# Kernel tuning notes

Measured on AMD Instinct MI355X. Metric: run time of the kernel, lower is better.

Reference implementation:

```python
import jax, jax.numpy as jnp
import numpy as np

B, S, D_TEXT, MAXF = 2, 1024, 384, 5
D_MODEL, N_HEADS, D_FF, L = 768, 12, 3072, 4
HEAD_DIM = D_MODEL // N_HEADS
EPS = 1e-6
NEG = -1e9


def _rms(x, g):
    return x * jax.lax.rsqrt(jnp.mean(x * x, axis=-1, keepdims=True) + EPS) * g


def _attn(x, w, mask):
    # w: [4, d, d] = (wq, wk, wv, wo); mask: [b, s, s] bool (True = attend)
    b, s, d = x.shape

    def proj(W):
        return jnp.einsum('bsd,de->bse', x, W).reshape(b, s, N_HEADS, HEAD_DIM).transpose(0, 2, 1, 3)

    q, k, v = proj(w[0]), proj(w[1]), proj(w[2])
    scale = jnp.asarray(1.0 / np.sqrt(HEAD_DIM), x.dtype)
    scores = jnp.einsum('bhqe,bhke->bhqk', q, k) * scale
    scores = jnp.where(mask[:, None], scores, NEG)
    p = jax.nn.softmax(scores, axis=-1)
    o = jnp.einsum('bhqk,bhke->bhqe', p, v).transpose(0, 2, 1, 3).reshape(b, s, d)
    return jnp.einsum('bsd,de->bse', o, w[3])


def _forward(number_values, datetime_values, boolean_values, text_values, column_name_values,
             W_cn, b_cn, W_num, b_num, W_text, b_text, W_dt, b_dt, W_bool, b_bool,
             g_cn, g_num, g_text, g_dt, g_bool, mask_emb,
             blk_norms, blk_attn, blk_up, blk_gate, blk_down,
             g_out, Wd_num, bd_num, Wd_dt, bd_dt, Wd_bool, bd_bool, Wd_text, bd_text,
             node_indices, table_name_indices, column_name_indices,
             f2p_neighbor_indices, semantic_types, masks, is_padding):
    valid = ~is_padding
    pv = valid[:, :, None] & valid[:, None, :]  # [b,s,s]
    eye = jnp.eye(S, dtype=bool)[None]
    same_node = node_indices[:, :, None] == node_indices[:, None, :]
    col_mask = ((column_name_indices[:, :, None] == column_name_indices[:, None, :])
                & (table_name_indices[:, :, None] == table_name_indices[:, None, :]) & pv) | eye
    feat_mask = (same_node & pv) | eye
    # kv node is one of q's f2p neighbors
    nei = (f2p_neighbor_indices[:, :, :, None] == node_indices[:, None, None, :]).any(axis=2)
    nei_mask = ((nei | same_node) & pv) | eye
    full_mask = pv | eye

    # per-semantic-type value encoders (Linear + RMSNorm)
    cn = _rms(column_name_values @ W_cn + b_cn, g_cn)
    num_e = _rms(number_values @ W_num + b_num, g_num)
    text_e = _rms(text_values @ W_text + b_text, g_text)
    dt_e = _rms(datetime_values @ W_dt + b_dt, g_dt)
    bool_e = _rms(boolean_values @ W_bool + b_bool, g_bool)
    st = semantic_types[..., None]
    val = jnp.where(st == 0, num_e, jnp.where(st == 1, text_e, jnp.where(st == 2, dt_e, bool_e)))
    # masked cells get the learned mask embedding for their semantic type
    val = jnp.where(masks[..., None], mask_emb[semantic_types], val)
    x = val + cn

    for i in range(L):
        nw, aw = blk_norms[i], blk_attn[i]
        x = x + _attn(_rms(x, nw[0]), aw[0], col_mask)
        x = x + _attn(_rms(x, nw[1]), aw[1], feat_mask)
        x = x + _attn(_rms(x, nw[2]), aw[2], nei_mask)
        x = x + _attn(_rms(x, nw[3]), aw[3], full_mask)
        h = _rms(x, nw[4])
        x = x + (jax.nn.silu(h @ blk_gate[i]) * (h @ blk_up[i])) @ blk_down[i]

    h = _rms(x, g_out)
    return (h @ Wd_num + bd_num, h @ Wd_dt + bd_dt, h @ Wd_bool + bd_bool, h @ Wd_text + bd_text)


def setup_inputs() -> dict:
    key = jax.random.key(0)
    ks = iter(jax.random.split(key, 64))

    def nrm(shape, scale=0.02):
        return jax.random.normal(next(ks), shape, jnp.float32) * scale

    inp = {}
    inp['number_values'] = jax.random.normal(next(ks), (B, S, 1), jnp.float32)
    inp['datetime_values'] = jax.random.normal(next(ks), (B, S, 1), jnp.float32)
    inp['boolean_values'] = jax.random.normal(next(ks), (B, S, 1), jnp.float32)
    inp['text_values'] = jax.random.normal(next(ks), (B, S, D_TEXT), jnp.float32)
    inp['column_name_values'] = jax.random.normal(next(ks), (B, S, D_TEXT), jnp.float32)
    inp['W_cn'] = nrm((D_TEXT, D_MODEL)); inp['b_cn'] = jnp.zeros((D_MODEL,), jnp.float32)
    inp['W_num'] = nrm((1, D_MODEL)); inp['b_num'] = jnp.zeros((D_MODEL,), jnp.float32)
    inp['W_text'] = nrm((D_TEXT, D_MODEL)); inp['b_text'] = jnp.zeros((D_MODEL,), jnp.float32)
    inp['W_dt'] = nrm((1, D_MODEL)); inp['b_dt'] = jnp.zeros((D_MODEL,), jnp.float32)
    inp['W_bool'] = nrm((1, D_MODEL)); inp['b_bool'] = jnp.zeros((D_MODEL,), jnp.float32)
    for n in ('g_cn', 'g_num', 'g_text', 'g_dt', 'g_bool'):
        inp[n] = jnp.ones((D_MODEL,), jnp.float32)
    inp['mask_emb'] = jax.random.normal(next(ks), (4, D_MODEL), jnp.float32)
    inp['blk_norms'] = jnp.ones((L, 5, D_MODEL), jnp.float32)
    inp['blk_attn'] = nrm((L, 4, 4, D_MODEL, D_MODEL))
    inp['blk_up'] = nrm((L, D_MODEL, D_FF))
    inp['blk_gate'] = nrm((L, D_MODEL, D_FF))
    inp['blk_down'] = nrm((L, D_FF, D_MODEL))
    inp['g_out'] = jnp.ones((D_MODEL,), jnp.float32)
    inp['Wd_num'] = nrm((D_MODEL, 1)); inp['bd_num'] = jnp.zeros((1,), jnp.float32)
    inp['Wd_dt'] = nrm((D_MODEL, 1)); inp['bd_dt'] = jnp.zeros((1,), jnp.float32)
    inp['Wd_bool'] = nrm((D_MODEL, 1)); inp['bd_bool'] = jnp.zeros((1,), jnp.float32)
    inp['Wd_text'] = nrm((D_MODEL, D_TEXT)); inp['bd_text'] = jnp.zeros((D_TEXT,), jnp.float32)
    inp['node_indices'] = jax.random.randint(next(ks), (B, S), 0, 128)
    inp['table_name_indices'] = jax.random.randint(next(ks), (B, S), 0, 8)
    inp['column_name_indices'] = jax.random.randint(next(ks), (B, S), 0, 32)
    inp['f2p_neighbor_indices'] = jax.random.randint(next(ks), (B, S, MAXF), 0, 128)
    inp['semantic_types'] = jax.random.randint(next(ks), (B, S), 0, 4)
    inp['masks'] = jax.random.bernoulli(next(ks), 0.15, (B, S))
    inp['is_padding'] = jnp.zeros((B, S), bool)
    return inp


def reference(number_values, datetime_values, boolean_values, text_values, column_name_values,
              W_cn, b_cn, W_num, b_num, W_text, b_text, W_dt, b_dt, W_bool, b_bool,
              g_cn, g_num, g_text, g_dt, g_bool, mask_emb,
              blk_norms, blk_attn, blk_up, blk_gate, blk_down,
              g_out, Wd_num, bd_num, Wd_dt, bd_dt, Wd_bool, bd_bool, Wd_text, bd_text,
              node_indices, table_name_indices, column_name_indices,
              f2p_neighbor_indices, semantic_types, masks, is_padding):
    return _forward(number_values, datetime_values, boolean_values, text_values, column_name_values,
                    W_cn, b_cn, W_num, b_num, W_text, b_text, W_dt, b_dt, W_bool, b_bool,
                    g_cn, g_num, g_text, g_dt, g_bool, mask_emb,
                    blk_norms, blk_attn, blk_up, blk_gate, blk_down,
                    g_out, Wd_num, bd_num, Wd_dt, bd_dt, Wd_bool, bd_bool, Wd_text, bd_text,
                    node_indices, table_name_indices, column_name_indices,
                    f2p_neighbor_indices, semantic_types, masks, is_padding)
```

## Files before the change

kernel.cpp:

```cpp
#include <hip/hip_runtime.h>
#include <hip/hip_bf16.h>
#include <cmath>
#include <stdint.h>


#define BB 2
#define SS 1024
#define DT 384
#define DM 768
#define NH 12
#define DH 64
#define DFF 3072
#define NL 4
#define NROW (BB*SS)
#define EPSF 1e-6f
#define QSC 0.1803368801111244f

typedef unsigned short u16;
typedef unsigned char u8;
typedef unsigned int u32;
typedef __attribute__((ext_vector_type(8))) short s16x8;
typedef __attribute__((ext_vector_type(4))) float f32x4;

__device__ __forceinline__ u16 f2bu(float f){
    u32 x = __float_as_uint(f);
    u32 r = (x + 0x7fffu + ((x>>16)&1u)) >> 16;
    return (u16)r;
}
__device__ __forceinline__ u32 pk2(float lo, float hi){
    return (u32)f2bu(lo) | ((u32)f2bu(hi)<<16);
}
__device__ __forceinline__ int swz(int row, int c){
    return (row<<6) + (((((c>>3) ^ row) & 7))<<3) + (c&7);
}
__device__ __forceinline__ float rsum16(float v){
    v += __shfl_xor(v,1); v += __shfl_xor(v,2);
    v += __shfl_xor(v,4); v += __shfl_xor(v,8);
    return v;
}
#define SBAR() __builtin_amdgcn_sched_barrier(0)
#define GLDS(src,dst) __builtin_amdgcn_global_load_lds((const __attribute__((address_space(1))) u32*)(src), (__attribute__((address_space(3))) u32*)(dst), 16, 0, 0)
#define GLDS4(src,dst) __builtin_amdgcn_global_load_lds((const __attribute__((address_space(1))) u32*)(src), (__attribute__((address_space(3))) u32*)(dst), 4, 0, 0)

__device__ void norm_bool_body(const void* __restrict__ src, u8* __restrict__ dst, int n)
{
    __shared__ int fl[4];
    if (threadIdx.x<4) fl[threadIdx.x]=0;
    __syncthreads();
    const u32* wsrc = (const u32*)src;
    const int nw = n/4;
    int any=0, nb=0, hi=0, lo=0;
    for (int i=threadIdx.x;i<nw;i+=blockDim.x){
        u32 v=wsrc[i];
        if (!v) continue;
        any=1;
        #pragma unroll
        for (int b=0;b<4;b++){
            u32 by=(v>>(8*b))&0xffu;
            if (by>1u) nb=1;
            if (by==1u && b!=0) hi=1;
        }
        if ((v&0xffffu)==0x3f80u) lo=1;
    }
    if (any) atomicOr(&fl[0],1);
    if (nb)  atomicOr(&fl[1],1);
    if (hi)  atomicOr(&fl[2],1);
    if (lo)  atomicOr(&fl[3],1);
    __syncthreads();
    int c;
    if (!fl[0]) c=0;
    else if (!fl[1]) c = fl[2] ? 2 : 1;
    else if (fl[3]) c = 3;
    else c = 1;
    for (int i=threadIdx.x;i<n;i+=blockDim.x){
        u8 v;
        if (c==0)      v=0;
        else if (c==1) v = (((const u32*)src)[i]!=0u);
        else if (c==2) v = (((const u8*)src)[i]!=0u);
        else           v = (((const u16*)src)[i]!=0u);
        dst[i]=v;
    }
}
__global__ void norm_bool2(const void* s0, u8* d0, const void* s1, u8* d1, int n)
{
    if (blockIdx.x==0) norm_bool_body(s0,d0,n);
    else               norm_bool_body(s1,d1,n);
}

__global__ void pack_meta(const int* __restrict__ node, const int* __restrict__ colx,
                          const int* __restrict__ tbl, const u8* __restrict__ pad,
                          u32* __restrict__ pm, int n, float* __restrict__ rsz, int nz)
{
    int i = blockIdx.x*256 + threadIdx.x;
    if (i<n)
        pm[i] = (u32)(node[i]&0xff) | ((u32)(colx[i]&0xff)<<8) | ((u32)(tbl[i]&0xff)<<16) | ((u32)(pad[i]&1)<<24);
    for (int z=i; z<nz; z+=gridDim.x*256) rsz[z]=0.f;
}

__global__ __launch_bounds__(256) void mask4_kernel(const u32* __restrict__ pm, const int* __restrict__ f2p,
                                                    u8* __restrict__ m4)
{
    const int b = blockIdx.y, kg = blockIdx.x;
    const int t = threadIdx.x;
    __shared__ u32 qm[1024];
    __shared__ int qf[1024*5];
    for (int i=t;i<1024;i+=256) qm[i] = pm[b*SS+i];
    for (int i=t;i<5*1024;i+=256) qf[i] = f2p[b*SS*5 + i];
    __syncthreads();
    const int q0 = t*4;
    u32 qmv[4]; int qn[4]; int qfv[4][5];
    #pragma unroll
    for (int j=0;j<4;j++){
        qmv[j]=qm[q0+j]; qn[j]=(int)(qmv[j]&0xffu);
        #pragma unroll
        for (int f=0;f<5;f++) qfv[j][f]=qf[(q0+j)*5+f];
    }
    for (int kk=0;kk<16;kk++){
        const int k = kg*16+kk;
        const u32 km = qm[k];
        const int kn = (int)(km&0xffu);
        u32 outw=0;
        #pragma unroll
        for (int j=0;j<4;j++){
            const u32 qmw = qmv[j];
            const bool pv = (((qmw|km)>>24)&1u)==0u;
            u32 by=0;
            if ((((qmw^km)&0x00ffff00u)==0u) && pv) by|=1;
            if ((((qmw^km)&0xffu)==0u) && pv) by|=2;
            bool nei = (qfv[j][0]==kn)||(qfv[j][1]==kn)||(qfv[j][2]==kn)||(qfv[j][3]==kn)||(qfv[j][4]==kn)
                       ||(qn[j]==kn);
            if (nei && pv) by|=4;
            if (pv) by|=8;
            if ((q0+j)==k) by=15;
            outw |= by<<(8*j);
        }
        ((u32*)(m4 + ((size_t)b<<20) + ((size_t)k<<10)))[t] = outw;
    }
}

__global__ void repack_mask(const u8* __restrict__ m4, u8* __restrict__ mbp)
{
    const int gid = blockIdx.x*256 + threadIdx.x;
    const int qb = gid & 127;
    const int bk = gid >> 7;
    const u8* src = m4 + ((size_t)bk<<10) + qb*8;
    u32 lo = *(const u32*)src, hi = *(const u32*)(src+4);
    u32 out[4] = {0,0,0,0};
    #pragma unroll
    for (int j=0;j<4;j++){
        u32 b0 = (lo>>(8*j)) & 0xffu;
        u32 b1 = (hi>>(8*j)) & 0xffu;
        #pragma unroll
        for (int tt=0;tt<4;tt++){
            out[tt] |= ((b0>>tt)&1u) << j;
            out[tt] |= ((b1>>tt)&1u) << (j+4);
        }
    }
    u8* dst = mbp + (size_t)bk*512 + qb;
    #pragma unroll
    for (int tt=0;tt<4;tt++) dst[tt*128] = (u8)out[tt];
}

__global__ __launch_bounds__(256) void transpose_cvt2(const float* __restrict__ src, u16* __restrict__ dst,
                                                      int K, int N, size_t dz,
                                                      const float* __restrict__ gbase, int gmode)
{
    const int z = blockIdx.z;
    src += (size_t)z*K*N;
    dst += (size_t)z*dz;
    const float* g = nullptr;
    if (gmode==1){ int m = z&3; if (m<3) g = gbase + (size_t)((z>>4)*5 + ((z>>2)&3))*768; }
    else if (gmode==2){ g = gbase + (size_t)z*5*768; }
    const int n0 = blockIdx.x*32, k0 = blockIdx.y*64;
    __shared__ float t[64][33];
    const int tid = threadIdx.x;
    const int kr = tid>>3, n4 = (tid&7)*4;
    #pragma unroll
    for (int p=0;p<2;p++){
        const int k = p*32 + kr;
        float gk = g ? g[k0+k] : 1.f;
        float4 v = *(const float4*)(src + (size_t)(k0+k)*N + n0 + n4);
        t[k][n4]=v.x*gk; t[k][n4+1]=v.y*gk; t[k][n4+2]=v.z*gk; t[k][n4+3]=v.w*gk;
    }
    __syncthreads();
    const int n = tid>>3, ks = (tid&7)*8;
    const int ng = n0 + n;
    uint4 o;
    u32* op = (u32*)&o;
    #pragma unroll
    for (int i=0;i<4;i++)
        op[i] = pk2(t[ks+2*i][n], t[ks+2*i+1][n]);
    *(uint4*)&dst[(((size_t)(ng>>7)*(K>>6) + (k0>>6))<<13) + ((ng&127)<<6) + ks] = o;
}

__global__ __launch_bounds__(256) void cvt_tiled2(const float* __restrict__ s0, u16* __restrict__ d0,
                                                  const float* __restrict__ s1, u16* __restrict__ d1, int K)
{
    const float* src = blockIdx.y ? s1 : s0;
    u16* dst = blockIdx.y ? d1 : d0;
    const int gid = blockIdx.x*256 + threadIdx.x;
    const int base = gid*8;
    const int row = base / K, col = base - row*K;
    float4 a = *(const float4*)(src + base);
    float4 b = *(const float4*)(src + base + 4);
    uint4 o;
    o.x = pk2(a.x,a.y); o.y = pk2(a.z,a.w);
    o.z = pk2(b.x,b.y); o.w = pk2(b.z,b.w);
    *(uint4*)&dst[(((size_t)(row>>7)*(K>>6) + (col>>6))<<13) + ((row&127)<<6) + (col&63)] = o;
}

__device__ __forceinline__ void stage3(const u16* aT, const u16* bT, int cb, int brow,
                                       u16* la, u16* lb, int w, int l)
{
    #pragma unroll
    for (int p=0;p<2;p++){
        const int q = p*256 + w*64 + l;
        const int row = q>>2, u = q&3;
        const int so = row*64 + cb + (((u ^ ((row>>1)&3))&3)<<3);
        GLDS(aT+so, la + p*2048 + w*512);
    }
    {
        const int q = w*64 + l;
        const int row = q>>2, u = q&3;
        const int so = (brow+row)*64 + cb + (((u ^ ((row>>1)&3))&3)<<3);
        GLDS(bT+so, lb + w*512);
    }
}

__global__ __launch_bounds__(256,3) void gemm_t(
    const u16* __restrict__ At, const u16* __restrict__ Bt,
    int K, int AMS, u16* __restrict__ qk16, u16* __restrict__ vt16,
    const float* __restrict__ rs_in)
{
    __shared__ u16 lds[4][6144];
    const int tid = threadIdx.x;
    const int lane = tid & 63, w = tid >> 6;
    const int cg = lane >> 4, cl = lane & 15;
    const int NT = K >> 5;
    const int n0 = blockIdx.x*64;
    const int brow = n0 & 64;
    const size_t bNb = (size_t)(n0>>7)*(K>>6);

    const u16* aB = At + ((size_t)blockIdx.y * AMS << 13);
    const u16* bB = Bt + (bNb << 13);

    f32x4 acc[2][4];
    #pragma unroll
    for (int i=0;i<2;i++)
        #pragma unroll
        for (int j=0;j<4;j++) acc[i][j] = (f32x4){0.f,0.f,0.f,0.f};

    stage3(aB, bB, 0,  brow, &lds[0][0], &lds[0][4096], w, lane);
    stage3(aB, bB, 32, brow, &lds[1][0], &lds[1][4096], w, lane);

    for (int kt=0; kt<NT; kt++){
        const int buf = kt & 3;
        if (kt+2 < NT){
            const int k2 = kt+2;
            stage3(aB + ((size_t)(k2>>1)<<13), bB + ((size_t)(k2>>1)<<13),
                   (k2&1)<<5, brow, &lds[k2&3][0], &lds[k2&3][4096], w, lane);
            asm volatile("s_waitcnt vmcnt(6)" ::: "memory");
        } else if (kt+1 < NT){
            asm volatile("s_waitcnt vmcnt(3)" ::: "memory");
        } else {
            asm volatile("s_waitcnt vmcnt(0)" ::: "memory");
        }
        SBAR(); __builtin_amdgcn_s_barrier(); SBAR();
        s16x8 af[2], bf[4];
        #pragma unroll
        for (int mt=0;mt<2;mt++){
            const int ra = w*32 + mt*16 + cl;
            af[mt] = *(const s16x8*)&lds[buf][ra*32 + (((cg ^ ((ra>>1)&3))&3)<<3)];
        }
        #pragma unroll
        for (int nt=0;nt<4;nt++){
            const int rb = nt*16 + cl;
            bf[nt] = *(const s16x8*)&lds[buf][4096 + rb*32 + (((cg ^ ((rb>>1)&3))&3)<<3)];
        }
        #pragma unroll
        for (int mt=0;mt<2;mt++)
            #pragma unroll
            for (int nt=0;nt<4;nt++)
                acc[mt][nt] = __builtin_amdgcn_mfma_f32_16x16x32_bf16(af[mt], bf[nt], acc[mt][nt], 0,0,0);
    }

    const int m0 = blockIdx.y*128;
    #pragma unroll
    for (int mt=0;mt<2;mt++){
        const int grow0 = m0 + w*32 + mt*16 + cg*4;
        float rr[4];
        #pragma unroll
        for (int j=0;j<4;j++) rr[j] = rsqrtf(rs_in[grow0+j]*(1.f/768.f) + EPSF);
        #pragma unroll
        for (int nt=0;nt<4;nt++){
            const int col = n0 + nt*16 + cl;
            if (col < 768){
                #pragma unroll
                for (int j=0;j<4;j++)
                    qk16[(size_t)(grow0+j)*1536 + col] = f2bu(acc[mt][nt][j]*rr[j]*QSC);
            } else if (col < 1536){
                #pragma unroll
                for (int j=0;j<4;j++)
                    qk16[(size_t)(grow0+j)*1536 + col] = f2bu(acc[mt][nt][j]*rr[j]);
            } else {
                const int b = grow0>>10, s0 = grow0&1023;
                const int dhg = col - 1536;
                uint2 o;
                o.x = pk2(acc[mt][nt][0]*rr[0], acc[mt][nt][1]*rr[1]);
                o.y = pk2(acc[mt][nt][2]*rr[2], acc[mt][nt][3]*rr[3]);
                *(uint2*)(vt16 + ((size_t)(b*768 + dhg)<<10) + s0) = o;
            }
        }
    }
}

__global__ __launch_bounds__(256,3) void gemm_gu(
    const u16* __restrict__ At, const u16* __restrict__ Bg, const u16* __restrict__ Bu,
    const float* __restrict__ rs_in, u16* __restrict__ o16)
{
    __shared__ u16 lds[3][8192];
    const int tid = threadIdx.x;
    const int lane = tid & 63, w = tid >> 6;
    const int cg = lane >> 4, cl = lane & 15;
    const int NT = 24;
    const int n0 = blockIdx.x*64;
    const int brow = n0 & 64;
    const size_t bNb = (size_t)(n0>>7)*12;

    const u16* aB = At + ((size_t)blockIdx.y * 12 << 13);
    const u16* gB = Bg + (bNb << 13);
    const u16* uB = Bu + (bNb << 13);

    f32x4 accg[2][4], accu[2][4];
    #pragma unroll
    for (int i=0;i<2;i++)
        #pragma unroll
        for (int j=0;j<4;j++){ accg[i][j] = (f32x4){0.f,0.f,0.f,0.f}; accu[i][j] = (f32x4){0.f,0.f,0.f,0.f}; }

    #define STAGE_GU(kt2, cb, buf) { \
        const u16* a_ = aB + ((size_t)(kt2)<<13); \
        const u16* g_ = gB + ((size_t)(kt2)<<13); \
        const u16* u_ = uB + ((size_t)(kt2)<<13); \
        _Pragma("unroll") \
        for (int p=0;p<2;p++){ \
            const int q = p*256 + w*64 + lane; \
            const int row = q>>2, uu = q&3; \
            const int so = row*64 + (cb) + (((uu ^ ((row>>1)&3))&3)<<3); \
            GLDS(a_+so, &lds[buf][0] + p*2048 + w*512); \
        } \
        { \
            const int q = w*64 + lane; \
            const int row = q>>2, uu = q&3; \
            const int so = (brow+row)*64 + (cb) + (((uu ^ ((row>>1)&3))&3)<<3); \
            GLDS(g_+so, &lds[buf][4096] + w*512); \
            GLDS(u_+so, &lds[buf][6144] + w*512); \
        } }

    STAGE_GU(0, 0, 0);

    for (int kt=0; kt<NT; kt++){
        const int buf = kt % 3;
        if (kt+1 < NT){
            const int k1 = kt+1;
            STAGE_GU(k1>>1, (k1&1)<<5, k1%3);
            asm volatile("s_waitcnt vmcnt(4)" ::: "memory");
        } else {
            asm volatile("s_waitcnt vmcnt(0)" ::: "memory");
        }
        SBAR(); __builtin_amdgcn_s_barrier(); SBAR();
        s16x8 af[2], bg[4], bu[4];
        #pragma unroll
        for (int mt=0;mt<2;mt++){
            const int ra = w*32 + mt*16 + cl;
            af[mt] = *(const s16x8*)&lds[buf][ra*32 + (((cg ^ ((ra>>1)&3))&3)<<3)];
        }
        #pragma unroll
        for (int nt=0;nt<4;nt++){
            const int rb = nt*16 + cl;
            const int sw = (((cg ^ ((rb>>1)&3))&3)<<3);
            bg[nt] = *(const s16x8*)&lds[buf][4096 + rb*32 + sw];
            bu[nt] = *(const s16x8*)&lds[buf][6144 + rb*32 + sw];
        }
        #pragma unroll
        for (int mt=0;mt<2;mt++)
            #pragma unroll
            for (int nt=0;nt<4;nt++){
                accg[mt][nt] = __builtin_amdgcn_mfma_f32_16x16x32_bf16(af[mt], bg[nt], accg[mt][nt], 0,0,0);
                accu[mt][nt] = __builtin_amdgcn_mfma_f32_16x16x32_bf16(af[mt], bu[nt], accu[mt][nt], 0,0,0);
            }
    }

    const int m0 = blockIdx.y*128;
    #pragma unroll
    for (int mt=0;mt<2;mt++){
        const int grow0 = m0 + w*32 + mt*16 + cg*4;
        float rr[4];
        #pragma unroll
        for (int j=0;j<4;j++) rr[j] = rsqrtf(rs_in[grow0+j]*(1.f/768.f) + EPSF);
        #pragma unroll
        for (int nt=0;nt<4;nt++){
            const int col = n0 + nt*16 + cl;
            const size_t tb = (((size_t)(grow0>>7)*48 + (col>>6))<<13) + (col&63);
            #pragma unroll
            for (int j=0;j<4;j++){
                float g = accg[mt][nt][j]*rr[j];
                float u = accu[mt][nt][j]*rr[j];
                float s = g/(1.f+__expf(-g))*u;
                o16[tb + (((grow0+j)&127)<<6)] = f2bu(s);
            }
        }
    }
}

__device__ __forceinline__ void stage64(const u16* aT, int arow, const u16* bT, int brow, int cb,
                                        u16* la, u16* lb, int w, int l)
{
    const int q = w*64 + l;
    const int row = q>>2, u = q&3;
    const int sw = (((u ^ ((row>>1)&3))&3)<<3);
    GLDS(aT + (arow+row)*64 + cb + sw, la + w*512);
    GLDS(bT + (brow+row)*64 + cb + sw, lb + w*512);
}

__global__ __launch_bounds__(256,4) void gemm_t64(
    const u16* __restrict__ At, const u16* __restrict__ Bt, float* __restrict__ C,
    int N, int K, int AMS, int flags, const float* __restrict__ bias,
    u16* __restrict__ o16, float* __restrict__ rs_out)
{
    __shared__ u16 lds[4][4096];
    const int tid = threadIdx.x;
    const int lane = tid & 63, w = tid >> 6;
    const int cg = lane >> 4, cl = lane & 15;
    const int NT = K >> 5;
    const int n0 = blockIdx.x*64;
    const int m0 = blockIdx.y*64;
    const int brow = n0 & 64, arow = m0 & 64;

    const u16* aB = At + ((size_t)(m0>>7) * AMS << 13);
    const u16* bB = Bt + ((size_t)(n0>>7) * (K>>6) << 13);

    f32x4 acc[4];
    #pragma unroll
    for (int j=0;j<4;j++) acc[j] = (f32x4){0.f,0.f,0.f,0.f};

    stage64(aB, arow, bB, brow, 0,  &lds[0][0], &lds[0][2048], w, lane);
    stage64(aB, arow, bB, brow, 32, &lds[1][0], &lds[1][2048], w, lane);

    for (int kt=0; kt<NT; kt++){
        const int buf = kt & 3;
        if (kt+2 < NT){
            const int k2 = kt+2;
            stage64(aB + ((size_t)(k2>>1)<<13), arow, bB + ((size_t)(k2>>1)<<13), brow,
                    (k2&1)<<5, &lds[k2&3][0], &lds[k2&3][2048], w, lane);
            asm volatile("s_waitcnt vmcnt(4)" ::: "memory");
        } else if (kt+1 < NT){
            asm volatile("s_waitcnt vmcnt(2)" ::: "memory");
        } else {
            asm volatile("s_waitcnt vmcnt(0)" ::: "memory");
        }
        SBAR(); __builtin_amdgcn_s_barrier(); SBAR();
        const int ra = w*16 + cl;
        s16x8 af = *(const s16x8*)&lds[buf][ra*32 + (((cg ^ ((ra>>1)&3))&3)<<3)];
        s16x8 bf[4];
        #pragma unroll
        for (int nt=0;nt<4;nt++){
            const int rb = nt*16 + cl;
            bf[nt] = *(const s16x8*)&lds[buf][2048 + rb*32 + (((cg ^ ((rb>>1)&3))&3)<<3)];
        }
        #pragma unroll
        for (int nt=0;nt<4;nt++)
            acc[nt] = __builtin_amdgcn_mfma_f32_16x16x32_bf16(af, bf[nt], acc[nt], 0,0,0);
    }

    const int grow0 = m0 + w*16 + cg*4;
    const bool do_acc = (flags&1), do_bias = (flags&2);
    float tmp[4][4];
    #pragma unroll
    for (int nt=0;nt<4;nt++){
        const int col = n0 + nt*16 + cl;
        float bv = do_bias ? bias[col] : 0.f;
        #pragma unroll
        for (int j=0;j<4;j++){
            float v = acc[nt][j] + bv;
            float* cp = C + (size_t)(grow0+j)*N + col;
            if (do_acc) v += *cp;
            *cp = v;
            tmp[nt][j] = v;
        }
    }
    if (o16){
        #pragma unroll
        for (int nt=0;nt<4;nt++){
            const int col = n0 + nt*16 + cl;
            const size_t tb = (((size_t)(grow0>>7)*12 + (col>>6))<<13) + (col&63);
            #pragma unroll
            for (int j=0;j<4;j++)
                o16[tb + (((grow0+j)&127)<<6)] = f2bu(tmp[nt][j]);
        }
    }
    if (rs_out){
        #pragma unroll
        for (int j=0;j<4;j++){
            float s = tmp[0][j]*tmp[0][j] + tmp[1][j]*tmp[1][j]
                    + tmp[2][j]*tmp[2][j] + tmp[3][j]*tmp[3][j];
            s = rsum16(s);
            if (cl==0) atomicAdd(rs_out + grow0 + j, s);
        }
    }
}

__global__ __launch_bounds__(256,2) void attn_mfma5(
    const u16* __restrict__ qk16, const u16* __restrict__ vt16,
    const u8* __restrict__ mbp, int mt,
    u16* __restrict__ ob16)
{
    const int bh = blockIdx.y;
    const int b = bh / NH, h = bh % NH;
    const int q0 = blockIdx.x * 64;
    const int tid = threadIdx.x;
    const int w = tid>>6, lane = tid&63, cg = lane>>4, cl = lane&15;
    const int srow = lane>>3;
    const int sseg = (lane&7) ^ srow;

    __shared__ u16 Ks[3][4096], Vt[3][4096], Ps[4096];
    __shared__ u8 Ms[3][512];

    s16x8 qa0, qa1;
    {
        const u16* qrow = qk16 + (size_t)(b*SS+q0 + w*16 + cl)*1536 + h*64;
        qa0 = *(const s16x8*)(qrow + cg*8);
        qa1 = *(const s16x8*)(qrow + 32 + cg*8);
        asm volatile("" :: "v"(*(const f32x4*)&qa0), "v"(*(const f32x4*)&qa1));
    }

    const u16* kbase = qk16 + (size_t)(b*SS)*1536 + 768 + h*64;
    const u16* vbase = vt16 + ((size_t)(b*768 + h*64)<<10);
    const u8* mrow0 = mbp + ((size_t)(b<<10))*512 + mt*128 + (q0>>3);

    #pragma unroll
    for (int p=0;p<2;p++){
        const int row = p*32 + w*8 + srow;
        GLDS(kbase + (size_t)row*1536 + sseg*8, Ks[0] + p*2048 + w*512);
        GLDS(vbase + ((size_t)row<<10) + sseg*8, Vt[0] + p*2048 + w*512);
    }
    if (lane < 32){
        const int krow = w*16 + (lane>>1);
        GLDS4(mrow0 + (size_t)krow*512 + (lane&1)*4, Ms[0] + w*128);
    }

    f32x4 o[4];
    #pragma unroll
    for (int nt=0;nt<4;nt++) o[nt] = (f32x4){0.f,0.f,0.f,0.f};
    float lsum[4] = {0.f,0.f,0.f,0.f};

    for (int kc=0;kc<16;kc++){
        const int buf = kc % 3;
        if (kc < 15){
            const int nb = (kc+1) % 3;
            const int kn0 = kc*64 + 64;
            #pragma unroll
            for (int p=0;p<2;p++){
                const int row = p*32 + w*8 + srow;
                GLDS(kbase + (size_t)(kn0+row)*1536 + sseg*8, Ks[nb] + p*2048 + w*512);
                GLDS(vbase + ((size_t)row<<10) + kn0 + sseg*8, Vt[nb] + p*2048 + w*512);
            }
            if (lane < 32){
                const int krow = kn0 + w*16 + (lane>>1);
                GLDS4(mrow0 + (size_t)krow*512 + (lane&1)*4, Ms[nb] + w*128);
            }
            asm volatile("s_waitcnt vmcnt(5)" ::: "memory");
        } else {
            asm volatile("s_waitcnt vmcnt(0)" ::: "memory");
        }
        SBAR(); __builtin_amdgcn_s_barrier(); SBAR();

        f32x4 sc[4];
        #pragma unroll
        for (int nt=0;nt<4;nt++) sc[nt] = (f32x4){0.f,0.f,0.f,0.f};
        __builtin_amdgcn_s_setprio(1);
        #pragma unroll
        for (int nt=0;nt<4;nt++){
            s16x8 kb0 = *(const s16x8*)&Ks[buf][swz(nt*16+cl, cg*8)];
            sc[nt] = __builtin_amdgcn_mfma_f32_16x16x32_bf16(qa0, kb0, sc[nt], 0,0,0);
        }
        #pragma unroll
        for (int nt=0;nt<4;nt++){
            s16x8 kb1 = *(const s16x8*)&Ks[buf][swz(nt*16+cl, 32+cg*8)];
            sc[nt] = __builtin_amdgcn_mfma_f32_16x16x32_bf16(qa1, kb1, sc[nt], 0,0,0);
        }
        __builtin_amdgcn_s_setprio(0);

        float pP[4][4];
        const int qb = 2*w + (cg>>1);
        const int bsh = (cg&1)*4;
        #pragma unroll
        for (int nt=0;nt<4;nt++){
            const u32 mrow = Ms[buf][(nt*16+cl)*8 + qb];
            #pragma unroll
            for (int j=0;j<4;j++){
                float pe = exp2f(fminf(sc[nt][j], 100.f));
                pe = ((mrow >> (bsh+j)) & 1u) ? pe : 0.f;
                pP[nt][j] = pe;
                lsum[j] += pe;
            }
        }

        #pragma unroll
        for (int nt=0;nt<4;nt++)
            #pragma unroll
            for (int j=0;j<4;j++)
                Ps[swz(w*16+cg*4+j, nt*16+cl)] = f2bu(pP[nt][j]);

        __builtin_amdgcn_s_setprio(1);
        #pragma unroll
        for (int ks=0;ks<2;ks++){
            s16x8 pa = *(const s16x8*)&Ps[swz(w*16+cl, ks*32+cg*8)];
            #pragma unroll
            for (int nt=0;nt<4;nt++){
                s16x8 vb = *(const s16x8*)&Vt[buf][swz(nt*16+cl, ks*32+cg*8)];
                o[nt] = __builtin_amdgcn_mfma_f32_16x16x32_bf16(pa, vb, o[nt], 0,0,0);
            }
        }
        __builtin_amdgcn_s_setprio(0);
    }

    #pragma unroll
    for (int j=0;j<4;j++){
        const float inv = 1.f/rsum16(lsum[j]);
        const int row = b*SS + q0 + w*16 + cg*4 + j;
        const size_t rb = ((size_t)(row>>7)*12 + h)*8192 + ((row&127)<<6);
        #pragma unroll
        for (int nt=0;nt<4;nt++)
            ob16[rb + nt*16 + cl] = f2bu(o[nt][j]*inv);
    }
}

__global__ __launch_bounds__(256) void fuse_encode(
    const float* __restrict__ cnbuf, const float* __restrict__ textbuf,
    const float* __restrict__ numv, const float* __restrict__ dtv, const float* __restrict__ boolv,
    const float* __restrict__ Wnum, const float* __restrict__ bnum,
    const float* __restrict__ Wdt, const float* __restrict__ bdt,
    const float* __restrict__ Wbool, const float* __restrict__ bbool,
    const float* __restrict__ gcn, const float* __restrict__ gnum, const float* __restrict__ gtext,
    const float* __restrict__ gdt, const float* __restrict__ gbool,
    const float* __restrict__ memb, const int* __restrict__ stypes, const u8* __restrict__ masks,
    float* __restrict__ x, u16* __restrict__ xt16, float* __restrict__ rs0)
{
    const int row = blockIdx.x;
    const int t = threadIdx.x;
    __shared__ float red[256];

    float cn3[3]; float ss=0.f;
    #pragma unroll
    for (int j=0;j<3;j++){
        cn3[j] = cnbuf[(size_t)row*DM + t + j*256];
        ss += cn3[j]*cn3[j];
    }
    red[t]=ss; __syncthreads();
    for (int s=128;s>0;s>>=1){ if(t<s) red[t]+=red[t+s]; __syncthreads(); }
    {
        float r = rsqrtf(red[0]/(float)DM + EPSF);
        #pragma unroll
        for (int j=0;j<3;j++) cn3[j] *= r*gcn[t+j*256];
    }
    __syncthreads();

    const int st = stypes[row];
    float val[3]; ss=0.f;
    if (st==1){
        #pragma unroll
        for (int j=0;j<3;j++){
            val[j] = textbuf[(size_t)row*DM + t + j*256];
            ss += val[j]*val[j];
        }
    } else {
        const float* Wp = (st==0)?Wnum:((st==2)?Wdt:Wbool);
        const float* bp = (st==0)?bnum:((st==2)?bdt:bbool);
        const float* vp = (st==0)?numv:((st==2)?dtv:boolv);
        float v = vp[row];
        #pragma unroll
        for (int j=0;j<3;j++){
            int e=t+j*256;
            val[j] = v*Wp[e] + bp[e];
            ss += val[j]*val[j];
        }
    }
    red[t]=ss; __syncthreads();
    for (int s=128;s>0;s>>=1){ if(t<s) red[t]+=red[t+s]; __syncthreads(); }
    const float* gp = (st==0)?gnum:((st==1)?gtext:((st==2)?gdt:gbool));
    float r2 = rsqrtf(red[0]/(float)DM + EPSF);
    bool mk = masks[row]!=0;
    float xv[3]; float sx=0.f;
    #pragma unroll
    for (int j=0;j<3;j++){
        int e=t+j*256;
        float vv = val[j]*r2*gp[e];
        if (mk) vv = memb[st*DM+e];
        xv[j] = vv + cn3[j];
        x[(size_t)row*DM+e] = xv[j];
        sx += xv[j]*xv[j];
    }
    __syncthreads();
    red[t]=sx; __syncthreads();
    for (int s=128;s>0;s>>=1){ if(t<s) red[t]+=red[t+s]; __syncthreads(); }
    if (t==0) rs0[row] = red[0];
    const size_t mb = (size_t)(row>>7)*12;
    const int rr = (row&127)<<6;
    #pragma unroll
    for (int j=0;j<3;j++){
        const int c = t + j*256;
        xt16[((mb + (c>>6))<<13) + rr + (c&63)] = f2bu(xv[j]);
    }
}

__global__ __launch_bounds__(256) void decode2(
    const float* __restrict__ x, const float* __restrict__ gout,
    const float* __restrict__ Wn, const float* __restrict__ bn,
    const float* __restrict__ Wd, const float* __restrict__ bd,
    const float* __restrict__ Wb, const float* __restrict__ bb,
    float* __restrict__ out, u16* __restrict__ h16)
{
    const int row = blockIdx.x;
    const int t = threadIdx.x;
    __shared__ float h[DM];
    __shared__ float red[256];
    const float* xr = x + (size_t)row*DM;
    float v0=xr[t], v1=xr[t+256], v2=xr[t+512];
    red[t]=v0*v0+v1*v1+v2*v2; __syncthreads();
    for (int s=128;s>0;s>>=1){ if(t<s) red[t]+=red[t+s]; __syncthreads(); }
    float r = rsqrtf(red[0]/(float)DM + EPSF);
    float h0 = v0*r*gout[t], h1 = v1*r*gout[t+256], h2 = v2*r*gout[t+512];
    h[t]=h0; h[t+256]=h1; h[t+512]=h2;
    const size_t mb = (size_t)(row>>7)*12;
    const int rr = (row&127)<<6;
    #pragma unroll
    for (int j=0;j<3;j++){
        const int c = t + j*256;
        const float v = (j==0?h0:(j==1?h1:h2));
        h16[((mb + (c>>6))<<13) + rr + (c&63)] = f2bu(v);
    }
    __syncthreads();

    float pn=0.f,pd=0.f,pb=0.f;
    for (int k=t;k<DM;k+=256){ float hv=h[k]; pn+=hv*Wn[k]; pd+=hv*Wd[k]; pb+=hv*Wb[k]; }
    red[t]=pn; __syncthreads();
    for (int s=128;s>0;s>>=1){ if(t<s) red[t]+=red[t+s]; __syncthreads(); }
    float tn=red[0]; __syncthreads();
    red[t]=pd; __syncthreads();
    for (int s=128;s>0;s>>=1){ if(t<s) red[t]+=red[t+s]; __syncthreads(); }
    float td=red[0]; __syncthreads();
    red[t]=pb; __syncthreads();
    for (int s=128;s>0;s>>=1){ if(t<s) red[t]+=red[t+s]; __syncthreads(); }
    float tb=red[0];
    if (t==0){
        out[row]          = tn + bn[0];
        out[NROW + row]   = td + bd[0];
        out[2*NROW + row] = tb + bb[0];
    }
}

extern "C" void kernel_launch(void* const* d_in, const int* in_sizes, int n_in,
                              void* d_out, int out_size, void* d_ws, size_t ws_size,
                              hipStream_t stream)
{
    const float* numv   = (const float*)d_in[0];
    const float* dtval  = (const float*)d_in[1];
    const float* boolv  = (const float*)d_in[2];
    const float* textv  = (const float*)d_in[3];
    const float* cnamev = (const float*)d_in[4];
    const float* Wcn=(const float*)d_in[5];  const float* bcn=(const float*)d_in[6];
    const float* Wnum=(const float*)d_in[7]; const float* bnum=(const float*)d_in[8];
    const float* Wtext=(const float*)d_in[9];const float* btext=(const float*)d_in[10];
    const float* Wdt=(const float*)d_in[11]; const float* bdt=(const float*)d_in[12];
    const float* Wbool=(const float*)d_in[13];const float* bbool=(const float*)d_in[14];
    const float* gcn=(const float*)d_in[15]; const float* gnum=(const float*)d_in[16];
    const float* gtext=(const float*)d_in[17];const float* gdt=(const float*)d_in[18];
    const float* gbool=(const float*)d_in[19];
    const float* memb=(const float*)d_in[20];
    const float* norms_all=(const float*)d_in[21];
    const float* attw_all=(const float*)d_in[22];
    const float* up_all=(const float*)d_in[23];
    const float* gate_all=(const float*)d_in[24];
    const float* down_all=(const float*)d_in[25];
    const float* gout=(const float*)d_in[26];
    const float* Wdn=(const float*)d_in[27]; const float* bdn=(const float*)d_in[28];
    const float* Wdd=(const float*)d_in[29]; const float* bdd=(const float*)d_in[30];
    const float* Wdb=(const float*)d_in[31]; const float* bdb=(const float*)d_in[32];
    const float* Wdtx=(const float*)d_in[33];const float* bdtx=(const float*)d_in[34];
    const int* node=(const int*)d_in[35];
    const int* tbl =(const int*)d_in[36];
    const int* colx=(const int*)d_in[37];
    const int* f2p =(const int*)d_in[38];
    const int* styp=(const int*)d_in[39];

    const size_t SA = (size_t)768*768;
    const size_t SG = (size_t)768*3072;
    const size_t SC = (size_t)384*768;
    const size_t NX = (size_t)NROW*DM;

    u8* base = (u8*)d_ws;
    float* x  = (float*)base;
    u16* xt16 = (u16*)(base + 6291456);
    u16* ob16 = (u16*)(base + 9437184);
    u16* qk16 = (u16*)(base + 12582912);
    u16* vt16 = (u16*)(base + 18874368);
    u16* gu16 = (u16*)(base + 22020096);
    u16* wA   = (u16*)(base + 47185920);
    u16* wGU  = wA + 64*SA;
    u16* wD   = wGU + 8*SG;
    u16* wCN  = wD + 4*SG;
    u16* wTX  = wCN + SC;
    u16* wDX  = wTX + SC;
    u8* nmask = (u8*)(wDX + SC);
    u8* npad  = nmask + NROW;
    u32* pmeta = (u32*)(npad + NROW + 64);
    float* rsbuf = (float*)(pmeta + NROW);
    u8* m4 = (u8*)(rsbuf + 21*2048);
    u8* mbp = m4 + ((size_t)2<<20);

    u16* cnT16   = qk16;
    u16* textT16 = vt16;
    float* cnbuf   = (float*)gu16;
    float* textbuf = cnbuf + NX;

    float* out = (float*)d_out;

    norm_bool2<<<2,256,0,stream>>>(d_in[40], nmask, d_in[41], npad, NROW);
    pack_meta<<<8,256,0,stream>>>(node, colx, tbl, npad, pmeta, NROW, rsbuf, 21*2048);
    mask4_kernel<<<dim3(64,2),256,0,stream>>>(pmeta, f2p, m4);
    repack_mask<<<1024,256,0,stream>>>(m4, mbp);

    transpose_cvt2<<<dim3(24,12,64),256,0,stream>>>(attw_all, wA, 768, 768, SA, norms_all, 1);
    transpose_cvt2<<<dim3(96,12,4),256,0,stream>>>(gate_all, wGU,      768, 3072, 2*SG, norms_all + 4*768, 2);
    transpose_cvt2<<<dim3(96,12,4),256,0,stream>>>(up_all,   wGU + SG, 768, 3072, 2*SG, norms_all + 4*768, 2);
    transpose_cvt2<<<dim3(24,48,4),256,0,stream>>>(down_all, wD, 3072, 768, SG, nullptr, 0);
    transpose_cvt2<<<dim3(24,6,1),256,0,stream>>>(Wcn,   wCN, 384, 768, 0, nullptr, 0);
    transpose_cvt2<<<dim3(24,6,1),256,0,stream>>>(Wtext, wTX, 384, 768, 0, nullptr, 0);
    transpose_cvt2<<<dim3(12,12,1),256,0,stream>>>(Wdtx, wDX, 768, 384, 0, nullptr, 0);

    cvt_tiled2<<<dim3(384,2),256,0,stream>>>(cnamev, cnT16, textv, textT16, 384);
    gemm_t64<<<dim3(12,32),256,0,stream>>>(cnT16,   wCN, cnbuf,   768, 384, 6, 2, bcn,   nullptr, nullptr);
    gemm_t64<<<dim3(12,32),256,0,stream>>>(textT16, wTX, textbuf, 768, 384, 6, 2, btext, nullptr, nullptr);
    fuse_encode<<<NROW,256,0,stream>>>(cnbuf, textbuf, numv, dtval, boolv,
        Wnum,bnum,Wdt,bdt,Wbool,bbool, gcn,gnum,gtext,gdt,gbool,
        memb, styp, nmask, x, xt16, rsbuf);

    const dim3 ga(SS/64, BB*NH);
    for (int l=0; l<NL; l++){
        for (int a=0; a<4; a++){
            const int slot = l*5 + a;
            const u16* wqkv = wA + (size_t)((l*4+a)*4)*SA;
            gemm_t<<<dim3(36,16),256,0,stream>>>(xt16, wqkv, 768, 12, qk16, vt16,
                rsbuf + (size_t)slot*2048);
            attn_mfma5<<<ga,256,0,stream>>>(qk16, vt16, mbp, a, ob16);
            gemm_t64<<<dim3(12,32),256,0,stream>>>(ob16, wqkv + 3*SA, x, 768, 768, 12, 1, nullptr,
                xt16, rsbuf + (size_t)(slot+1)*2048);
        }
        gemm_gu<<<dim3(48,16),256,0,stream>>>(xt16, wGU + (size_t)l*2*SG, wGU + (size_t)l*2*SG + SG,
            rsbuf + (size_t)(l*5+4)*2048, gu16);
        gemm_t64<<<dim3(12,32),256,0,stream>>>(gu16, wD + (size_t)l*SG, x, 768, 3072, 48, 1, nullptr,
            xt16, rsbuf + (size_t)((l+1)*5)*2048);
    }

    decode2<<<NROW,256,0,stream>>>(x, gout, Wdn,bdn, Wdd,bdd, Wdb,bdb, out, xt16);
    gemm_t64<<<dim3(6,32),256,0,stream>>>(xt16, wDX, out + 3*NROW, 384, 768, 12, 2, bdtx,
        nullptr, nullptr);
}
```

Measured before the change: 1.345 ms.

## Fuse mask bit-packing into mask kernel and deepen gate/up GEMM prefetch

The mask kernel now bit-packs its per-query mask bytes directly into the bit-plane layout, using a lane shuffle to merge neighbouring threads' words. This removes the separate repack kernel and the 2 MB intermediate mask buffer round-trip. Separately, the gate/up GEMM now prefetches two k-tiles ahead in its triple buffer instead of one, and adds a trailing barrier to protect buffer reuse. The deeper prefetch hides more load latency but costs an extra barrier on every iteration.

```diff
diff --git a/kernel.cpp b/kernel.cpp
--- a/kernel.cpp
+++ b/kernel.cpp
@@ -98,7 +98,7 @@
 }
 
 __global__ __launch_bounds__(256) void mask4_kernel(const u32* __restrict__ pm, const int* __restrict__ f2p,
-                                                    u8* __restrict__ m4)
+                                                    u8* __restrict__ mbp)
 {
     const int b = blockIdx.y, kg = blockIdx.x;
     const int t = threadIdx.x;
@@ -115,6 +115,8 @@
         #pragma unroll
         for (int f=0;f<5;f++) qfv[j][f]=qf[(q0+j)*5+f];
     }
+    const int qb = t>>1;
+    const bool hiHalf = (t&1);
     for (int kk=0;kk<16;kk++){
         const int k = kg*16+kk;
         const u32 km = qm[k];
@@ -134,31 +136,21 @@
             if ((q0+j)==k) by=15;
             outw |= by<<(8*j);
         }
-        ((u32*)(m4 + ((size_t)b<<20) + ((size_t)k<<10)))[t] = outw;
-    }
-}
-
-__global__ void repack_mask(const u8* __restrict__ m4, u8* __restrict__ mbp)
-{
-    const int gid = blockIdx.x*256 + threadIdx.x;
-    const int qb = gid & 127;
-    const int bk = gid >> 7;
-    const u8* src = m4 + ((size_t)bk<<10) + qb*8;
-    u32 lo = *(const u32*)src, hi = *(const u32*)(src+4);
-    u32 out[4] = {0,0,0,0};
-    #pragma unroll
-    for (int j=0;j<4;j++){
-        u32 b0 = (lo>>(8*j)) & 0xffu;
-        u32 b1 = (hi>>(8*j)) & 0xffu;
-        #pragma unroll
-        for (int tt=0;tt<4;tt++){
-            out[tt] |= ((b0>>tt)&1u) << j;
-            out[tt] |= ((b1>>tt)&1u) << (j+4);
-        }
-    }
-    u8* dst = mbp + (size_t)bk*512 + qb;
-    #pragma unroll
-    for (int tt=0;tt<4;tt++) dst[tt*128] = (u8)out[tt];
+        const u32 pw = __shfl_xor(outw, 1);
+        if (!hiHalf){
+            u8* dst = mbp + ((size_t)((b<<10)+k))*512 + qb;
+            #pragma unroll
+            for (int tt=0;tt<4;tt++){
+                u32 lo4=0, hi4=0;
+                #pragma unroll
+                for (int j=0;j<4;j++){
+                    lo4 |= ((outw>>(8*j+tt))&1u) << j;
+                    hi4 |= ((pw  >>(8*j+tt))&1u) << j;
+                }
+                dst[tt*128] = (u8)(lo4 | (hi4<<4));
+            }
+        }
+    }
 }
 
 __global__ __launch_bounds__(256) void transpose_cvt2(const float* __restrict__ src, u16* __restrict__ dst,
@@ -356,13 +348,16 @@
             GLDS(u_+so, &lds[buf][6144] + w*512); \
         } }
 
-    STAGE_GU(0, 0, 0);
+    STAGE_GU(0, 0,  0);
+    STAGE_GU(0, 32, 1);
 
     for (int kt=0; kt<NT; kt++){
         const int buf = kt % 3;
-        if (kt+1 < NT){
-            const int k1 = kt+1;
-            STAGE_GU(k1>>1, (k1&1)<<5, k1%3);
+        if (kt+2 < NT){
+            const int k2 = kt+2;
+            STAGE_GU(k2>>1, (k2&1)<<5, k2%3);
+            asm volatile("s_waitcnt vmcnt(8)" ::: "memory");
+        } else if (kt+1 < NT){
             asm volatile("s_waitcnt vmcnt(4)" ::: "memory");
         } else {
             asm volatile("s_waitcnt vmcnt(0)" ::: "memory");
@@ -388,6 +383,7 @@
                 accg[mt][nt] = __builtin_amdgcn_mfma_f32_16x16x32_bf16(af[mt], bg[nt], accg[mt][nt], 0,0,0);
                 accu[mt][nt] = __builtin_amdgcn_mfma_f32_16x16x32_bf16(af[mt], bu[nt], accu[mt][nt], 0,0,0);
             }
+        SBAR(); __builtin_amdgcn_s_barrier(); SBAR();
     }
 
     const int m0 = blockIdx.y*128;
@@ -815,8 +811,7 @@
     u8* npad  = nmask + NROW;
     u32* pmeta = (u32*)(npad + NROW + 64);
     float* rsbuf = (float*)(pmeta + NROW);
-    u8* m4 = (u8*)(rsbuf + 21*2048);
-    u8* mbp = m4 + ((size_t)2<<20);
+    u8* mbp = (u8*)(rsbuf + 21*2048);
 
     u16* cnT16   = qk16;
     u16* textT16 = vt16;
@@ -827,8 +822,7 @@
 
     norm_bool2<<<2,256,0,stream>>>(d_in[40], nmask, d_in[41], npad, NROW);
     pack_meta<<<8,256,0,stream>>>(node, colx, tbl, npad, pmeta, NROW, rsbuf, 21*2048);
-    mask4_kernel<<<dim3(64,2),256,0,stream>>>(pmeta, f2p, m4);
-    repack_mask<<<1024,256,0,stream>>>(m4, mbp);
+    mask4_kernel<<<dim3(64,2),256,0,stream>>>(pmeta, f2p, mbp);
 
     transpose_cvt2<<<dim3(24,12,64),256,0,stream>>>(attw_all, wA, 768, 768, SA, norms_all, 1);
     transpose_cvt2<<<dim3(96,12,4),256,0,stream>>>(gate_all, wGU,      768, 3072, 2*SG, norms_all + 4*768, 2);
```

Result: no change. 1.349 ms (+0.3%).
